# Optimization experiments

Hardware: AMD Instinct MI355X
Metric: run time of the kernel (lower is better)

## Reference

```python
import jax, jax.numpy as jnp
import numpy as np

NUM_CLASSES = 91
NUM_ANCHORS = 3234
VAR_XY, VAR_WH = 0.1, 0.2
SCORE_THRESH = 0.05
NMS_THRESH = 0.5
PRE_NMS_TOPK = 200  # original default 400; reduced to bound the [C-1,K,K] IoU buffer
MAX_DET = 100
BATCH = 64


def _xyxy_to_cxcywh(b):
    wh = b[..., 2:] - b[..., :2]
    c = b[..., :2] + 0.5 * wh
    return jnp.concatenate([c, wh], axis=-1)


def _pairwise_iou(b):
    # b: [K,4] xyxy -> [K,K] IoU
    lt = jnp.maximum(b[:, None, :2], b[None, :, :2])
    rb = jnp.minimum(b[:, None, 2:], b[None, :, 2:])
    inter = jnp.prod(jnp.clip(rb - lt, 0.0), axis=-1)
    area = jnp.prod(jnp.clip(b[:, 2:] - b[:, :2], 0.0), axis=-1)
    union = area[:, None] + area[None, :] - inter
    return inter / jnp.maximum(union, 1e-9)


def _nms_keep(boxes):
    # boxes [K,4] already sorted by descending score; greedy NMS keep mask [K]
    K = boxes.shape[0]
    iou = _pairwise_iou(jax.lax.stop_gradient(boxes))
    idx = jnp.arange(K)

    def body(i, keep):
        suppress = keep[i] & (iou[i] > NMS_THRESH) & (idx > i)
        return keep & ~suppress

    return jax.lax.fori_loop(0, K, body, jnp.ones((K,), dtype=bool))


def setup_inputs() -> dict:
    key = jax.random.key(0)
    k1, k2, k3, k4 = jax.random.split(key, 4)
    cls_logits = jax.random.normal(k1, (BATCH, NUM_ANCHORS, NUM_CLASSES), dtype=jnp.float32)
    box_reg = jax.random.normal(k2, (BATCH, NUM_ANCHORS, 4), dtype=jnp.float32)
    # valid normalized anchor boxes in xyxy
    cxy = jax.random.uniform(k3, (NUM_ANCHORS, 2), minval=0.05, maxval=0.95)
    wh = jax.random.uniform(k4, (NUM_ANCHORS, 2), minval=0.02, maxval=0.4)
    priors = jnp.concatenate([cxy - wh / 2, cxy + wh / 2], axis=-1).astype(jnp.float32)
    return {"cls_logits": cls_logits, "box_reg": box_reg, "priors": priors}


def reference(cls_logits, box_reg, priors):
    probs = jax.nn.softmax(cls_logits, axis=-1)           # [B,A,C]
    pr_c = _xyxy_to_cxcywh(priors)                        # [A,4]

    def per_image(args):
        loc, p = args                                     # [A,4], [A,C]
        # _decode with variances (0.1, 0.2)
        xy = loc[:, :2] * VAR_XY * pr_c[:, 2:] + pr_c[:, :2]
        wh = jnp.exp(loc[:, 2:] * VAR_WH) * pr_c[:, 2:]
        boxes = jnp.concatenate([xy - wh / 2, xy + wh / 2], axis=-1)  # [A,4]

        scores_c = p[:, 1:].T                             # [C-1, A], skip background
        vals, idx = jax.lax.top_k(scores_c, PRE_NMS_TOPK)  # [C-1,K] sorted desc
        boxes_c = boxes[idx]                              # [C-1,K,4]
        keep = jax.vmap(_nms_keep)(boxes_c)               # [C-1,K]
        valid = vals > SCORE_THRESH
        fscores = jnp.where(keep & valid, vals, 0.0)      # masked-out dets scored 0
        labels = jnp.broadcast_to(
            jnp.arange(1, NUM_CLASSES, dtype=jnp.float32)[:, None], fscores.shape)

        flat_s = fscores.reshape(-1)
        flat_b = boxes_c.reshape(-1, 4)
        flat_l = labels.reshape(-1)
        top_s, top_i = jax.lax.top_k(flat_s, MAX_DET)     # global top-100 by score
        preds = jnp.concatenate(
            [flat_b[top_i], top_s[:, None], flat_l[top_i, None]], axis=-1)  # [100,6]
        return jnp.where(top_s[:, None] > 0, preds, 0.0)  # zero padding rows

    return jax.lax.map(per_image, (box_reg, probs))        # [B,100,6]
```

## Files before the change

kernel.cpp:

```cpp
#include <hip/hip_runtime.h>
#include <cstdint>

#define NCLS 91
#define NA   3234
#define NB   64
#define KTOP 200
#define CAP  128
#define MAXDET 100
#define NCM1 90
#define CAPI 8192
#define LCAP 256
#define NBIN 1024
#define BOFF 0x3D4C
#define FBUF 1024
#define PBLK 6468

typedef unsigned long long u64;
typedef unsigned int u32;


__device__ __forceinline__ u64 u64max(u64 a, u64 b) { return a > b ? a : b; }
__device__ __forceinline__ u64 u64min(u64 a, u64 b) { return a < b ? a : b; }

__device__ __forceinline__ u64 shfl_xor_u64(u64 v, int m) {
  int lo = __shfl_xor((int)(u32)v, m, 64);
  int hi = __shfl_xor((int)(u32)(v >> 32), m, 64);
  return ((u64)(u32)hi << 32) | (u32)lo;
}

template <int SLOTS>
__device__ __forceinline__ void bitonic_desc(u64* key, int t) {
  const int N = SLOTS * 64;
  for (int k = 2; k <= N; k <<= 1) {
    for (int j = k >> 1; j > 0; j >>= 1) {
      if (j >= 64) {
        int sj = j >> 6;
        #pragma unroll
        for (int s = 0; s < SLOTS; ++s) {
          int sp = s ^ sj;
          if (sp > s) {
            int e = s * 64 + t;
            bool up = ((e & k) == 0);
            u64 a = key[s], b = key[sp];
            u64 mx = u64max(a, b), mn = u64min(a, b);
            key[s]  = up ? mx : mn;
            key[sp] = up ? mn : mx;
          }
        }
      } else {
        #pragma unroll
        for (int s = 0; s < SLOTS; ++s) {
          int e = s * 64 + t;
          u64 p = shfl_xor_u64(key[s], j);
          bool up = ((e & k) == 0);
          bool lower = ((t & j) == 0);
          key[s] = (up == lower) ? u64max(key[s], p) : u64min(key[s], p);
        }
      }
    }
  }
}

__global__ __launch_bounds__(64) void prep_kernel(
    const float* __restrict__ logits, const float* __restrict__ box_reg,
    const float* __restrict__ priors, float* __restrict__ boxes,
    u64* __restrict__ cand, int* __restrict__ cnt) {
  __shared__ u64 lkey[LCAP];
  __shared__ unsigned short lbc[LCAP];
  __shared__ int lcnt;
  int t = threadIdx.x;
  if (t == 0) lcnt = 0;
  asm volatile("s_waitcnt lgkmcnt(0)" ::: "memory");
  __builtin_amdgcn_sched_barrier(0);

  int half = t & 1;
  int rloc = t >> 1;
  int i = blockIdx.x * 32 + rloc;
  int b = i / NA, a = i - b * NA;

  int F0   = half ? 45 : 0;
  int cntf = half ? 46 : 45;
  const float* lp = logits + (size_t)i * NCLS;
  const float* base = lp + F0;
  int g0 = (int)(((u32)(i * NCLS + F0)) & 3u);
  int lead = (4 - g0) & 3;
  int rem = cntf - lead;
  int n4 = rem >> 2;
  int tail = rem & 3;

  float lv0 = 0.f, lv1 = 0.f, lv2 = 0.f;
  if (lead > 0) lv0 = base[0];
  if (lead > 1) lv1 = base[1];
  if (lead > 2) lv2 = base[2];
  const float4* cv = (const float4*)(base + lead);
  float4 r[11];
  #pragma unroll
  for (int v = 0; v < 10; ++v) r[v] = cv[v];
  r[10] = make_float4(0.f, 0.f, 0.f, 0.f);
  if (n4 > 10) r[10] = cv[10];
  int toff = lead + 4 * n4;
  float tv0 = 0.f, tv1 = 0.f, tv2 = 0.f;
  if (tail > 0) tv0 = base[toff];
  if (tail > 1) tv1 = base[toff + 1];
  if (tail > 2) tv2 = base[toff + 2];

  if (!half) {
    float4 pr = ((const float4*)priors)[a];
    float pw = pr.z - pr.x, ph = pr.w - pr.y;
    float cx = pr.x + 0.5f * pw, cy = pr.y + 0.5f * ph;
    float4 lc = ((const float4*)box_reg)[i];
    float x = lc.x * 0.1f * pw + cx;
    float y = lc.y * 0.1f * ph + cy;
    float bw = expf(lc.z * 0.2f) * pw;
    float bh = expf(lc.w * 0.2f) * ph;
    float4 bxo;
    bxo.x = x - bw * 0.5f; bxo.y = y - bh * 0.5f;
    bxo.z = x + bw * 0.5f; bxo.w = y + bh * 0.5f;
    ((float4*)boxes)[i] = bxo;
  }

  float m = -3.402823466e38f;
  if (lead > 0) m = fmaxf(m, lv0);
  if (lead > 1) m = fmaxf(m, lv1);
  if (lead > 2) m = fmaxf(m, lv2);
  #pragma unroll
  for (int v = 0; v < 10; ++v) {
    float4 q = r[v];
    m = fmaxf(m, fmaxf(fmaxf(q.x, q.y), fmaxf(q.z, q.w)));
  }
  if (n4 > 10) {
    float4 q = r[10];
    m = fmaxf(m, fmaxf(fmaxf(q.x, q.y), fmaxf(q.z, q.w)));
  }
  if (tail > 0) m = fmaxf(m, tv0);
  if (tail > 1) m = fmaxf(m, tv1);
  if (tail > 2) m = fmaxf(m, tv2);
  m = fmaxf(m, __shfl_xor(m, 1, 64));

  auto FOLD = [&](float s) -> float {
    if (lead > 0) s += expf(lv0 - m);
    if (lead > 1) s += expf(lv1 - m);
    if (lead > 2) s += expf(lv2 - m);
    #pragma unroll
    for (int v = 0; v < 10; ++v) {
      float4 q = r[v];
      s += expf(q.x - m); s += expf(q.y - m);
      s += expf(q.z - m); s += expf(q.w - m);
    }
    if (n4 > 10) {
      float4 q = r[10];
      s += expf(q.x - m); s += expf(q.y - m);
      s += expf(q.z - m); s += expf(q.w - m);
    }
    if (tail > 0) s += expf(tv0 - m);
    if (tail > 1) s += expf(tv1 - m);
    if (tail > 2) s += expf(tv2 - m);
    return s;
  };

  float s = 0.f;
  if (!half) s = FOLD(0.f);
  float s_recv = __shfl_xor(s, 1, 64);
  if (half) s = FOLD(s_recv);
  float fin = __shfl_xor(s, 1, 64);
  float ssum = half ? s : fin;

  float lthr = logf(0.05f * ssum);
  u64 abits = (u64)(u32)(~a);
  int bb90 = b * NCM1;
  #define PUSH(L, CC) do { \
    float _d = (L) - m; \
    if (_d > lthr) { \
      float _e = expf(_d); \
      int _lp = atomicAdd(&lcnt, 1); \
      if (_lp < LCAP) { \
        lkey[_lp] = ((u64)__float_as_uint(_e / ssum) << 32) | abits; \
        lbc[_lp] = (unsigned short)(bb90 + (CC) - 1); \
      } \
    } \
  } while (0)

  if (lead > 0 && F0 != 0) PUSH(lv0, F0);
  if (lead > 1) PUSH(lv1, F0 + 1);
  if (lead > 2) PUSH(lv2, F0 + 2);
  {
    int c0 = F0 + lead;
    float4 q = r[0];
    if (c0 != 0) PUSH(q.x, c0);
    PUSH(q.y, c0 + 1); PUSH(q.z, c0 + 2); PUSH(q.w, c0 + 3);
  }
  #pragma unroll
  for (int v = 1; v < 10; ++v) {
    float4 q = r[v];
    int cb = F0 + lead + 4 * v;
    PUSH(q.x, cb); PUSH(q.y, cb + 1); PUSH(q.z, cb + 2); PUSH(q.w, cb + 3);
  }
  if (n4 > 10) {
    float4 q = r[10];
    int cb = F0 + lead + 40;
    PUSH(q.x, cb); PUSH(q.y, cb + 1); PUSH(q.z, cb + 2); PUSH(q.w, cb + 3);
  }
  {
    int cb = F0 + toff;
    if (tail > 0) PUSH(tv0, cb);
    if (tail > 1) PUSH(tv1, cb + 1);
    if (tail > 2) PUSH(tv2, cb + 2);
  }
  #undef PUSH

  asm volatile("s_waitcnt lgkmcnt(0)" ::: "memory");
  __builtin_amdgcn_sched_barrier(0);
  int nL = lcnt; if (nL > LCAP) nL = LCAP;
  for (int j = t; j < nL; j += 64) {
    int bcv = lbc[j];
    int pos = atomicAdd(&cnt[bcv], 1);
    if (pos < CAP) cand[(size_t)bcv * CAP + pos] = lkey[j];
  }
}

__global__ __launch_bounds__(256) void sort_nms_kernel(
    const u64* __restrict__ cand, const int* __restrict__ cnt,
    const float* __restrict__ boxes,
    u64* __restrict__ img_keys, int* __restrict__ img_cnt) {
  __shared__ float4 sbx[4][CAP];
  __shared__ float sar[4][CAP];
  __shared__ u64 sm[4][CAP][2];
  int w = threadIdx.x >> 6;
  int t = threadIdx.x & 63;
  int bc = blockIdx.x * 4 + w;
  int b = bc / NCM1;
  int cm1 = bc - b * NCM1;

  int n = cnt[bc]; if (n > CAP) n = CAP;

  u64 key[2];
  #pragma unroll
  for (int s = 0; s < 2; ++s) {
    int e = s * 64 + t;
    key[s] = (e < n) ? cand[(size_t)bc * CAP + e] : 0ULL;
  }
  if (n <= 64) bitonic_desc<1>(key, t);
  else         bitonic_desc<2>(key, t);

  #pragma unroll
  for (int s = 0; s < 2; ++s) {
    int rr = s * 64 + t;
    if (rr < n) {
      int a = (int)(~(u32)key[s]);
      float4 bbx = ((const float4*)boxes)[b * NA + a];
      sbx[w][rr] = bbx;
      sar[w][rr] = fmaxf(bbx.z - bbx.x, 0.f) * fmaxf(bbx.w - bbx.y, 0.f);
    }
  }
  __syncthreads();

  #pragma unroll
  for (int T = 0; T < 2; ++T) {
    int rr = T * 64 + t;
    float4 bi; float ai = 0.f;
    bool act = (rr < n);
    if (act) { bi = sbx[w][rr]; ai = sar[w][rr]; }
    u64 m0 = 0, m1 = 0;
    for (int j = T * 64 + 1; j < n; ++j) {
      float4 bj = sbx[w][j];
      float aj = sar[w][j];
      if (act && j > rr) {
        float xx1 = fmaxf(bi.x, bj.x), yy1 = fmaxf(bi.y, bj.y);
        float xx2 = fminf(bi.z, bj.z), yy2 = fminf(bi.w, bj.w);
        float inter = fmaxf(xx2 - xx1, 0.f) * fmaxf(yy2 - yy1, 0.f);
        float iou = inter / fmaxf(ai + aj - inter, 1e-9f);
        if (iou > 0.5f) {
          if (j < 64) m0 |= 1ull << j;
          else        m1 |= 1ull << (j - 64);
        }
      }
    }
    if (act) { sm[w][rr][0] = m0; sm[w][rr][1] = m1; }
  }
  __syncthreads();

  u64 kp0 = ~0ull, kp1 = ~0ull;
  for (int i = 0; i < n; ++i) {
    u64 s0 = sm[w][i][0], s1 = sm[w][i][1];
    u64 kw = (i < 64) ? kp0 : kp1;
    u64 live = 0ull - ((kw >> (i & 63)) & 1ull);
    kp0 &= ~(s0 & live); kp1 &= ~(s1 & live);
  }

  auto rng = [](int mm, int wd) -> u64 {
    int c = mm - wd * 64;
    if (c <= 0) return 0ull;
    if (c >= 64) return ~0ull;
    return (1ull << c) - 1ull;
  };
  u64 k0 = kp0 & rng(n, 0), k1 = kp1 & rng(n, 1);
  int c0 = __popcll(k0), c1 = __popcll(k1);
  int tot = c0 + c1;
  int base = 0;
  if (t == 0 && tot) base = atomicAdd(&img_cnt[b], tot);
  base = __shfl(base, 0, 64);
  if (tot) {
    u64 lmlt = (1ull << t) - 1ull;
    u64 kws[2] = {k0, k1};
    int pres[2] = {0, c0};
    #pragma unroll
    for (int s = 0; s < 2; ++s) {
      int rr = s * 64 + t;
      if (rr < n && ((kws[s] >> t) & 1ull)) {
        int pos = base + pres[s] + __popcll(kws[s] & lmlt);
        if (pos < CAPI) {
          u32 sbits = (u32)(key[s] >> 32);
          int fidx = cm1 * KTOP + rr;
          int anch = (int)(~(u32)key[s]);
          img_keys[(size_t)b * CAPI + pos] =
              ((u64)sbits << 27) | ((u64)(u32)(0x7FFF - fidx) << 12) | (u64)(u32)anch;
        }
      }
    }
  }
}

__global__ __launch_bounds__(1024) void topdet_kernel(
    const u64* __restrict__ img_keys, const int* __restrict__ img_cnt,
    const float* __restrict__ boxes, float* __restrict__ out) {
  __shared__ int hist[NBIN];
  __shared__ u64 buf[FBUF];
  __shared__ int sh_nsel, sh_T;
  int b = blockIdx.x, t = threadIdx.x;
  int n = img_cnt[b]; if (n > CAPI) n = CAPI;

  for (int i = t; i < NBIN; i += 1024) hist[i] = 0;
  if (t == 0) { sh_nsel = 0; sh_T = 0; }
  __syncthreads();

  for (int i = t; i < n; i += 1024) {
    int bin = (int)(img_keys[(size_t)b * CAPI + i] >> 43) - BOFF;
    bin = bin < 0 ? 0 : (bin > NBIN - 1 ? NBIN - 1 : bin);
    atomicAdd(&hist[bin], 1);
  }
  __syncthreads();

  if (t < 64) {
    int hi = NBIN - 1 - (t << 4);
    int cs = 0;
    #pragma unroll
    for (int k = 0; k < 16; ++k) cs += hist[hi - k];
    int cum = cs;
    for (int d = 1; d < 64; d <<= 1) {
      int o = __shfl_up(cum, d, 64);
      if (t >= d) cum += o;
    }
    int pre = cum - cs;
    if (pre < MAXDET && cum >= MAXDET) {
      int acc = pre;
      for (int k = 0; k < 16; ++k) {
        acc += hist[hi - k];
        if (acc >= MAXDET) { sh_T = hi - k; break; }
      }
    }
  }
  __syncthreads();

  int T = sh_T;
  for (int i = t; i < n; i += 1024) {
    u64 key = img_keys[(size_t)b * CAPI + i];
    int bin = (int)(key >> 43) - BOFF;
    bin = bin < 0 ? 0 : (bin > NBIN - 1 ? NBIN - 1 : bin);
    if (bin >= T) {
      int pos = atomicAdd(&sh_nsel, 1);
      if (pos < FBUF) buf[pos] = key;
    }
  }
  __syncthreads();

  int ns = sh_nsel; if (ns > FBUF) ns = FBUF;

  if (ns <= 256) {
    if (t < 64) {
      u64 key[4];
      #pragma unroll
      for (int s = 0; s < 4; ++s) {
        int e = s * 64 + t;
        key[s] = (e < ns) ? buf[e] : 0ULL;
      }
      if (ns <= 128) bitonic_desc<2>(key, t);
      else           bitonic_desc<4>(key, t);
      buf[t] = key[0];
      if (t < 36) buf[64 + t] = key[1];
    }
    __syncthreads();
  } else {
    int npow = 1; while (npow < ns) npow <<= 1;
    for (int i = t; i < npow; i += 1024) if (i >= ns) buf[i] = 0ULL;
    __syncthreads();
    for (int k = 2; k <= npow; k <<= 1) {
      for (int j = k >> 1; j > 0; j >>= 1) {
        for (int i = t; i < npow; i += 1024) {
          int l = i ^ j;
          if (l > i) {
            u64 x0 = buf[i], x1 = buf[l];
            bool up = ((i & k) == 0);
            if (up ? (x0 < x1) : (x0 > x1)) { buf[i] = x1; buf[l] = x0; }
          }
        }
        __syncthreads();
      }
    }
  }

  if (t < MAXDET) {
    float* row = out + ((size_t)b * MAXDET + t) * 6;
    if (t < ns) {
      u64 key = buf[t];
      float vsc = __uint_as_float((u32)(key >> 27));
      int fidx = 0x7FFF - (int)((key >> 12) & 0x7FFF);
      int a = (int)(key & 0xFFF);
      float4 bb = ((const float4*)boxes)[b * NA + a];
      row[0] = bb.x; row[1] = bb.y; row[2] = bb.z; row[3] = bb.w;
      row[4] = vsc;
      row[5] = (float)(fidx / KTOP + 1);
    } else {
      row[0] = 0.f; row[1] = 0.f; row[2] = 0.f;
      row[3] = 0.f; row[4] = 0.f; row[5] = 0.f;
    }
  }
}

extern "C" void kernel_launch(void* const* d_in, const int* in_sizes, int n_in,
                              void* d_out, int out_size, void* d_ws, size_t ws_size,
                              hipStream_t stream) {
  const float* logits  = (const float*)d_in[0];
  const float* box_reg = (const float*)d_in[1];
  const float* priors  = (const float*)d_in[2];
  float* out = (float*)d_out;

  char* ws = (char*)d_ws;
  size_t off = 0;
  float* boxes = (float*)(ws + off);               off += (size_t)NB * NA * 4 * sizeof(float);
  u64* cand = (u64*)(ws + off);                    off += (size_t)NB * NCM1 * CAP * sizeof(u64);
  u64* img_keys = (u64*)(ws + off);                off += (size_t)NB * CAPI * sizeof(u64);
  int* cnt = (int*)(ws + off);                     off += (size_t)NB * NCM1 * sizeof(int);
  int* img_cnt = (int*)(ws + off);                 off += (size_t)NB * sizeof(int);
  (void)ws_size; (void)in_sizes; (void)n_in; (void)out_size;

  hipMemsetAsync(cnt, 0, (size_t)(NB * NCM1 + NB) * sizeof(int), stream);
  prep_kernel<<<PBLK, 64, 0, stream>>>(
      logits, box_reg, priors, boxes, cand, cnt);
  sort_nms_kernel<<<NB * NCM1 / 4, 256, 0, stream>>>(
      cand, cnt, boxes, img_keys, img_cnt);
  topdet_kernel<<<NB, 1024, 0, stream>>>(img_keys, img_cnt, boxes, out);
}
```

Before: 225.9 us.

## Stage logits via async global-to-LDS loads, process two slabs per block

The prep kernel now has each 64-thread block handle two 32-anchor slabs. Logits are copied with global_load_lds directly into shared memory, and the second slab's load overlaps processing of the first. Each exp is computed once and reused for both the softmax sum and the candidate push, and box decode is spread across all 64 lanes. The cost is more LDS per block and half as many blocks, which may reduce occupancy and latency hiding. Correctness also relies on the hand-written vmcnt waits being placed right.

```diff
diff --git a/kernel.cpp b/kernel.cpp
--- a/kernel.cpp
+++ b/kernel.cpp
@@ -13,7 +13,6 @@
 #define NBIN 1024
 #define BOFF 0x3D4C
 #define FBUF 1024
-#define PBLK 6468
 
 typedef unsigned long long u64;
 typedef unsigned int u32;
@@ -61,152 +60,190 @@
   }
 }
 
+__device__ __forceinline__ void process_slab(
+    const float* sl, int slab, int t,
+    u64* lkey, unsigned short* lbc, int* lcnt) {
+  int half = t & 1;
+  int r = t >> 1;
+  int i = slab * 32 + r;
+  int b = i / NA, a = i - b * NA;
+
+  int F0 = half ? 45 : 0;
+  int cntf = half ? 46 : 45;
+  const float* base = sl + r * 91 + F0;
+  int g0 = (int)((u32)(r * 91 + F0) & 3u);
+  int lead = (4 - g0) & 3;
+  int rem = cntf - lead;
+  int n4 = rem >> 2;
+  int tail = rem & 3;
+
+  float lv0 = 0.f, lv1 = 0.f, lv2 = 0.f;
+  if (lead > 0) lv0 = base[0];
+  if (lead > 1) lv1 = base[1];
+  if (lead > 2) lv2 = base[2];
+  const float4* cv = (const float4*)(base + lead);
+  float4 r4[11];
+  #pragma unroll
+  for (int v = 0; v < 10; ++v) r4[v] = cv[v];
+  r4[10] = make_float4(0.f, 0.f, 0.f, 0.f);
+  if (n4 > 10) r4[10] = cv[10];
+  int toff = lead + 4 * n4;
+  float tv0 = 0.f, tv1 = 0.f, tv2 = 0.f;
+  if (tail > 0) tv0 = base[toff];
+  if (tail > 1) tv1 = base[toff + 1];
+  if (tail > 2) tv2 = base[toff + 2];
+
+  float m = -3.402823466e38f;
+  if (lead > 0) m = fmaxf(m, lv0);
+  if (lead > 1) m = fmaxf(m, lv1);
+  if (lead > 2) m = fmaxf(m, lv2);
+  #pragma unroll
+  for (int v = 0; v < 10; ++v) {
+    float4 q = r4[v];
+    m = fmaxf(m, fmaxf(fmaxf(q.x, q.y), fmaxf(q.z, q.w)));
+  }
+  if (n4 > 10) {
+    float4 q = r4[10];
+    m = fmaxf(m, fmaxf(fmaxf(q.x, q.y), fmaxf(q.z, q.w)));
+  }
+  if (tail > 0) m = fmaxf(m, tv0);
+  if (tail > 1) m = fmaxf(m, tv1);
+  if (tail > 2) m = fmaxf(m, tv2);
+  m = fmaxf(m, __shfl_xor(m, 1, 64));
+
+  float el0 = expf(lv0 - m), el1 = expf(lv1 - m), el2 = expf(lv2 - m);
+  float4 er[11];
+  #pragma unroll
+  for (int v = 0; v < 11; ++v) {
+    er[v].x = expf(r4[v].x - m);
+    er[v].y = expf(r4[v].y - m);
+    er[v].z = expf(r4[v].z - m);
+    er[v].w = expf(r4[v].w - m);
+  }
+  float et0 = expf(tv0 - m), et1 = expf(tv1 - m), et2 = expf(tv2 - m);
+
+  auto CHAIN = [&](float s) -> float {
+    if (lead > 0) s += el0;
+    if (lead > 1) s += el1;
+    if (lead > 2) s += el2;
+    #pragma unroll
+    for (int v = 0; v < 10; ++v) {
+      s += er[v].x; s += er[v].y; s += er[v].z; s += er[v].w;
+    }
+    if (n4 > 10) { s += er[10].x; s += er[10].y; s += er[10].z; s += er[10].w; }
+    if (tail > 0) s += et0;
+    if (tail > 1) s += et1;
+    if (tail > 2) s += et2;
+    return s;
+  };
+  float s = 0.f;
+  if (!half) s = CHAIN(0.f);
+  float s_recv = __shfl_xor(s, 1, 64);
+  if (half) s = CHAIN(s_recv);
+  float fin = __shfl_xor(s, 1, 64);
+  float ssum = half ? s : fin;
+
+  float lthr = logf(0.05f * ssum);
+  u64 abits = (u64)(u32)(~a);
+  int bb90 = b * NCM1;
+  #define PUSH(L, E, CC) do { \
+    if ((L) - m > lthr) { \
+      float _e = (E); \
+      int _lp = atomicAdd(lcnt, 1); \
+      if (_lp < LCAP) { \
+        lkey[_lp] = ((u64)__float_as_uint(_e / ssum) << 32) | abits; \
+        lbc[_lp] = (unsigned short)(bb90 + (CC) - 1); \
+      } \
+    } \
+  } while (0)
+
+  if (lead > 0 && F0 != 0) PUSH(lv0, el0, F0);
+  if (lead > 1) PUSH(lv1, el1, F0 + 1);
+  if (lead > 2) PUSH(lv2, el2, F0 + 2);
+  {
+    int c0 = F0 + lead;
+    if (c0 != 0) PUSH(r4[0].x, er[0].x, c0);
+    PUSH(r4[0].y, er[0].y, c0 + 1);
+    PUSH(r4[0].z, er[0].z, c0 + 2);
+    PUSH(r4[0].w, er[0].w, c0 + 3);
+  }
+  #pragma unroll
+  for (int v = 1; v < 10; ++v) {
+    int cb = F0 + lead + 4 * v;
+    PUSH(r4[v].x, er[v].x, cb);
+    PUSH(r4[v].y, er[v].y, cb + 1);
+    PUSH(r4[v].z, er[v].z, cb + 2);
+    PUSH(r4[v].w, er[v].w, cb + 3);
+  }
+  if (n4 > 10) {
+    int cb = F0 + lead + 40;
+    PUSH(r4[10].x, er[10].x, cb);
+    PUSH(r4[10].y, er[10].y, cb + 1);
+    PUSH(r4[10].z, er[10].z, cb + 2);
+    PUSH(r4[10].w, er[10].w, cb + 3);
+  }
+  {
+    int cb = F0 + toff;
+    if (tail > 0) PUSH(tv0, et0, cb);
+    if (tail > 1) PUSH(tv1, et1, cb + 1);
+    if (tail > 2) PUSH(tv2, et2, cb + 2);
+  }
+  #undef PUSH
+}
+
 __global__ __launch_bounds__(64) void prep_kernel(
     const float* __restrict__ logits, const float* __restrict__ box_reg,
     const float* __restrict__ priors, float* __restrict__ boxes,
     u64* __restrict__ cand, int* __restrict__ cnt) {
+  __shared__ __align__(16) float sl[2][2912];
   __shared__ u64 lkey[LCAP];
   __shared__ unsigned short lbc[LCAP];
   __shared__ int lcnt;
   int t = threadIdx.x;
   if (t == 0) lcnt = 0;
   asm volatile("s_waitcnt lgkmcnt(0)" ::: "memory");
+
+  int i2 = blockIdx.x * 64 + t;
+  int b2 = i2 / NA, a2 = i2 - b2 * NA;
+  float4 pr = ((const float4*)priors)[a2];
+  float4 lc = ((const float4*)box_reg)[i2];
+
+  #pragma unroll
+  for (int p = 0; p < 2; ++p) {
+    const float* gs = logits + (size_t)(blockIdx.x * 2 + p) * 2912;
+    #pragma unroll
+    for (int k = 0; k < 11; ++k) {
+      __builtin_amdgcn_global_load_lds(
+          (const __attribute__((address_space(1))) void*)(gs + k * 256 + t * 4),
+          (__attribute__((address_space(3))) void*)(&sl[p][k * 256]),
+          16, 0, 0);
+    }
+    if (t < 24) {
+      __builtin_amdgcn_global_load_lds(
+          (const __attribute__((address_space(1))) void*)(gs + 11 * 256 + t * 4),
+          (__attribute__((address_space(3))) void*)(&sl[p][11 * 256]),
+          16, 0, 0);
+    }
+  }
+
+  float pw = pr.z - pr.x, ph = pr.w - pr.y;
+  float cx = pr.x + 0.5f * pw, cy = pr.y + 0.5f * ph;
+  float x = lc.x * 0.1f * pw + cx;
+  float y = lc.y * 0.1f * ph + cy;
+  float bw = expf(lc.z * 0.2f) * pw;
+  float bh = expf(lc.w * 0.2f) * ph;
+  float4 bxo;
+  bxo.x = x - bw * 0.5f; bxo.y = y - bh * 0.5f;
+  bxo.z = x + bw * 0.5f; bxo.w = y + bh * 0.5f;
+  ((float4*)boxes)[i2] = bxo;
+
+  asm volatile("s_waitcnt vmcnt(12)" ::: "memory");
   __builtin_amdgcn_sched_barrier(0);
-
-  int half = t & 1;
-  int rloc = t >> 1;
-  int i = blockIdx.x * 32 + rloc;
-  int b = i / NA, a = i - b * NA;
-
-  int F0   = half ? 45 : 0;
-  int cntf = half ? 46 : 45;
-  const float* lp = logits + (size_t)i * NCLS;
-  const float* base = lp + F0;
-  int g0 = (int)(((u32)(i * NCLS + F0)) & 3u);
-  int lead = (4 - g0) & 3;
-  int rem = cntf - lead;
-  int n4 = rem >> 2;
-  int tail = rem & 3;
-
-  float lv0 = 0.f, lv1 = 0.f, lv2 = 0.f;
-  if (lead > 0) lv0 = base[0];
-  if (lead > 1) lv1 = base[1];
-  if (lead > 2) lv2 = base[2];
-  const float4* cv = (const float4*)(base + lead);
-  float4 r[11];
-  #pragma unroll
-  for (int v = 0; v < 10; ++v) r[v] = cv[v];
-  r[10] = make_float4(0.f, 0.f, 0.f, 0.f);
-  if (n4 > 10) r[10] = cv[10];
-  int toff = lead + 4 * n4;
-  float tv0 = 0.f, tv1 = 0.f, tv2 = 0.f;
-  if (tail > 0) tv0 = base[toff];
-  if (tail > 1) tv1 = base[toff + 1];
-  if (tail > 2) tv2 = base[toff + 2];
-
-  if (!half) {
-    float4 pr = ((const float4*)priors)[a];
-    float pw = pr.z - pr.x, ph = pr.w - pr.y;
-    float cx = pr.x + 0.5f * pw, cy = pr.y + 0.5f * ph;
-    float4 lc = ((const float4*)box_reg)[i];
-    float x = lc.x * 0.1f * pw + cx;
-    float y = lc.y * 0.1f * ph + cy;
-    float bw = expf(lc.z * 0.2f) * pw;
-    float bh = expf(lc.w * 0.2f) * ph;
-    float4 bxo;
-    bxo.x = x - bw * 0.5f; bxo.y = y - bh * 0.5f;
-    bxo.z = x + bw * 0.5f; bxo.w = y + bh * 0.5f;
-    ((float4*)boxes)[i] = bxo;
-  }
-
-  float m = -3.402823466e38f;
-  if (lead > 0) m = fmaxf(m, lv0);
-  if (lead > 1) m = fmaxf(m, lv1);
-  if (lead > 2) m = fmaxf(m, lv2);
-  #pragma unroll
-  for (int v = 0; v < 10; ++v) {
-    float4 q = r[v];
-    m = fmaxf(m, fmaxf(fmaxf(q.x, q.y), fmaxf(q.z, q.w)));
-  }
-  if (n4 > 10) {
-    float4 q = r[10];
-    m = fmaxf(m, fmaxf(fmaxf(q.x, q.y), fmaxf(q.z, q.w)));
-  }
-  if (tail > 0) m = fmaxf(m, tv0);
-  if (tail > 1) m = fmaxf(m, tv1);
-  if (tail > 2) m = fmaxf(m, tv2);
-  m = fmaxf(m, __shfl_xor(m, 1, 64));
-
-  auto FOLD = [&](float s) -> float {
-    if (lead > 0) s += expf(lv0 - m);
-    if (lead > 1) s += expf(lv1 - m);
-    if (lead > 2) s += expf(lv2 - m);
-    #pragma unroll
-    for (int v = 0; v < 10; ++v) {
-      float4 q = r[v];
-      s += expf(q.x - m); s += expf(q.y - m);
-      s += expf(q.z - m); s += expf(q.w - m);
-    }
-    if (n4 > 10) {
-      float4 q = r[10];
-      s += expf(q.x - m); s += expf(q.y - m);
-      s += expf(q.z - m); s += expf(q.w - m);
-    }
-    if (tail > 0) s += expf(tv0 - m);
-    if (tail > 1) s += expf(tv1 - m);
-    if (tail > 2) s += expf(tv2 - m);
-    return s;
-  };
-
-  float s = 0.f;
-  if (!half) s = FOLD(0.f);
-  float s_recv = __shfl_xor(s, 1, 64);
-  if (half) s = FOLD(s_recv);
-  float fin = __shfl_xor(s, 1, 64);
-  float ssum = half ? s : fin;
-
-  float lthr = logf(0.05f * ssum);
-  u64 abits = (u64)(u32)(~a);
-  int bb90 = b * NCM1;
-  #define PUSH(L, CC) do { \
-    float _d = (L) - m; \
-    if (_d > lthr) { \
-      float _e = expf(_d); \
-      int _lp = atomicAdd(&lcnt, 1); \
-      if (_lp < LCAP) { \
-        lkey[_lp] = ((u64)__float_as_uint(_e / ssum) << 32) | abits; \
-        lbc[_lp] = (unsigned short)(bb90 + (CC) - 1); \
-      } \
-    } \
-  } while (0)
-
-  if (lead > 0 && F0 != 0) PUSH(lv0, F0);
-  if (lead > 1) PUSH(lv1, F0 + 1);
-  if (lead > 2) PUSH(lv2, F0 + 2);
-  {
-    int c0 = F0 + lead;
-    float4 q = r[0];
-    if (c0 != 0) PUSH(q.x, c0);
-    PUSH(q.y, c0 + 1); PUSH(q.z, c0 + 2); PUSH(q.w, c0 + 3);
-  }
-  #pragma unroll
-  for (int v = 1; v < 10; ++v) {
-    float4 q = r[v];
-    int cb = F0 + lead + 4 * v;
-    PUSH(q.x, cb); PUSH(q.y, cb + 1); PUSH(q.z, cb + 2); PUSH(q.w, cb + 3);
-  }
-  if (n4 > 10) {
-    float4 q = r[10];
-    int cb = F0 + lead + 40;
-    PUSH(q.x, cb); PUSH(q.y, cb + 1); PUSH(q.z, cb + 2); PUSH(q.w, cb + 3);
-  }
-  {
-    int cb = F0 + toff;
-    if (tail > 0) PUSH(tv0, cb);
-    if (tail > 1) PUSH(tv1, cb + 1);
-    if (tail > 2) PUSH(tv2, cb + 2);
-  }
-  #undef PUSH
+  process_slab(&sl[0][0], blockIdx.x * 2, t, lkey, lbc, &lcnt);
+
+  asm volatile("s_waitcnt vmcnt(0)" ::: "memory");
+  __builtin_amdgcn_sched_barrier(0);
+  process_slab(&sl[1][0], blockIdx.x * 2 + 1, t, lkey, lbc, &lcnt);
 
   asm volatile("s_waitcnt lgkmcnt(0)" ::: "memory");
   __builtin_amdgcn_sched_barrier(0);
@@ -444,7 +481,7 @@
   (void)ws_size; (void)in_sizes; (void)n_in; (void)out_size;
 
   hipMemsetAsync(cnt, 0, (size_t)(NB * NCM1 + NB) * sizeof(int), stream);
-  prep_kernel<<<PBLK, 64, 0, stream>>>(
+  prep_kernel<<<NB * NA / 64, 64, 0, stream>>>(
       logits, box_reg, priors, boxes, cand, cnt);
   sort_nms_kernel<<<NB * NCM1 / 4, 256, 0, stream>>>(
       cand, cnt, boxes, img_keys, img_cnt);
```

After: 239.2 us. 1.06x slower.

## Run per-class greedy NMS wave-locally with shuffles and ballots instead of shared IoU matrix

Applied to the files above, without the earlier changes.

Drops the shared-memory box buffers and the full pairwise IoU bitmask matrix, along with both block barriers, from the sort/NMS kernel. Each lane now keeps its own one or two sorted boxes in registers. The wave walks candidates in score order, broadcasting each still-kept box with shuffles and suppressing later boxes via ballots. Suppressed candidates are skipped entirely, and freeing the shared memory should help occupancy. The trade-off is a serial per-candidate loop of shuffles and divisions instead of fully parallel IoU computation.

```diff
diff --git a/kernel.cpp b/kernel.cpp
--- a/kernel.cpp
+++ b/kernel.cpp
@@ -222,9 +222,6 @@
     const u64* __restrict__ cand, const int* __restrict__ cnt,
     const float* __restrict__ boxes,
     u64* __restrict__ img_keys, int* __restrict__ img_cnt) {
-  __shared__ float4 sbx[4][CAP];
-  __shared__ float sar[4][CAP];
-  __shared__ u64 sm[4][CAP][2];
   int w = threadIdx.x >> 6;
   int t = threadIdx.x & 63;
   int bc = blockIdx.x * 4 + w;
@@ -242,49 +239,18 @@
   if (n <= 64) bitonic_desc<1>(key, t);
   else         bitonic_desc<2>(key, t);
 
-  #pragma unroll
-  for (int s = 0; s < 2; ++s) {
-    int rr = s * 64 + t;
-    if (rr < n) {
-      int a = (int)(~(u32)key[s]);
-      float4 bbx = ((const float4*)boxes)[b * NA + a];
-      sbx[w][rr] = bbx;
-      sar[w][rr] = fmaxf(bbx.z - bbx.x, 0.f) * fmaxf(bbx.w - bbx.y, 0.f);
-    }
-  }
-  __syncthreads();
-
-  #pragma unroll
-  for (int T = 0; T < 2; ++T) {
-    int rr = T * 64 + t;
-    float4 bi; float ai = 0.f;
-    bool act = (rr < n);
-    if (act) { bi = sbx[w][rr]; ai = sar[w][rr]; }
-    u64 m0 = 0, m1 = 0;
-    for (int j = T * 64 + 1; j < n; ++j) {
-      float4 bj = sbx[w][j];
-      float aj = sar[w][j];
-      if (act && j > rr) {
-        float xx1 = fmaxf(bi.x, bj.x), yy1 = fmaxf(bi.y, bj.y);
-        float xx2 = fminf(bi.z, bj.z), yy2 = fminf(bi.w, bj.w);
-        float inter = fmaxf(xx2 - xx1, 0.f) * fmaxf(yy2 - yy1, 0.f);
-        float iou = inter / fmaxf(ai + aj - inter, 1e-9f);
-        if (iou > 0.5f) {
-          if (j < 64) m0 |= 1ull << j;
-          else        m1 |= 1ull << (j - 64);
-        }
-      }
-    }
-    if (act) { sm[w][rr][0] = m0; sm[w][rr][1] = m1; }
-  }
-  __syncthreads();
-
-  u64 kp0 = ~0ull, kp1 = ~0ull;
-  for (int i = 0; i < n; ++i) {
-    u64 s0 = sm[w][i][0], s1 = sm[w][i][1];
-    u64 kw = (i < 64) ? kp0 : kp1;
-    u64 live = 0ull - ((kw >> (i & 63)) & 1ull);
-    kp0 &= ~(s0 & live); kp1 &= ~(s1 & live);
+  float4 bx0 = make_float4(0.f, 0.f, 0.f, 0.f);
+  float4 bx1 = make_float4(0.f, 0.f, 0.f, 0.f);
+  float ar0 = 0.f, ar1 = 0.f;
+  if (t < n) {
+    int a = (int)(~(u32)key[0]);
+    bx0 = ((const float4*)boxes)[b * NA + a];
+    ar0 = fmaxf(bx0.z - bx0.x, 0.f) * fmaxf(bx0.w - bx0.y, 0.f);
+  }
+  if (64 + t < n) {
+    int a = (int)(~(u32)key[1]);
+    bx1 = ((const float4*)boxes)[b * NA + a];
+    ar1 = fmaxf(bx1.z - bx1.x, 0.f) * fmaxf(bx1.w - bx1.y, 0.f);
   }
 
   auto rng = [](int mm, int wd) -> u64 {
@@ -293,7 +259,45 @@
     if (c >= 64) return ~0ull;
     return (1ull << c) - 1ull;
   };
-  u64 k0 = kp0 & rng(n, 0), k1 = kp1 & rng(n, 1);
+  u64 kp0 = rng(n, 0), kp1 = rng(n, 1);
+  bool has1 = (n > 64);
+
+  for (int i = 0; i < n; ++i) {
+    bool hi = i >= 64;
+    u64 kw = hi ? kp1 : kp0;
+    if (!((kw >> (i & 63)) & 1ull)) continue;
+    int src = i & 63;
+    float bix = __shfl(hi ? bx1.x : bx0.x, src, 64);
+    float biy = __shfl(hi ? bx1.y : bx0.y, src, 64);
+    float biz = __shfl(hi ? bx1.z : bx0.z, src, 64);
+    float biw = __shfl(hi ? bx1.w : bx0.w, src, 64);
+    float ai  = __shfl(hi ? ar1 : ar0, src, 64);
+    if (!hi) {
+      float xx1 = fmaxf(bix, bx0.x), yy1 = fmaxf(biy, bx0.y);
+      float xx2 = fminf(biz, bx0.z), yy2 = fminf(biw, bx0.w);
+      float inter = fmaxf(xx2 - xx1, 0.f) * fmaxf(yy2 - yy1, 0.f);
+      float iou = inter / fmaxf(ai + ar0 - inter, 1e-9f);
+      u64 sup0 = __ballot(iou > 0.5f);
+      kp0 &= ~(sup0 & ~((2ull << i) - 1ull));
+      if (has1) {
+        float xx1b = fmaxf(bix, bx1.x), yy1b = fmaxf(biy, bx1.y);
+        float xx2b = fminf(biz, bx1.z), yy2b = fminf(biw, bx1.w);
+        float interb = fmaxf(xx2b - xx1b, 0.f) * fmaxf(yy2b - yy1b, 0.f);
+        float ioub = interb / fmaxf(ai + ar1 - interb, 1e-9f);
+        u64 sup1 = __ballot(ioub > 0.5f);
+        kp1 &= ~sup1;
+      }
+    } else {
+      float xx1b = fmaxf(bix, bx1.x), yy1b = fmaxf(biy, bx1.y);
+      float xx2b = fminf(biz, bx1.z), yy2b = fminf(biw, bx1.w);
+      float interb = fmaxf(xx2b - xx1b, 0.f) * fmaxf(yy2b - yy1b, 0.f);
+      float ioub = interb / fmaxf(ai + ar1 - interb, 1e-9f);
+      u64 sup1 = __ballot(ioub > 0.5f);
+      kp1 &= ~(sup1 & ~((2ull << (i - 64)) - 1ull));
+    }
+  }
+
+  u64 k0 = kp0, k1 = kp1;
   int c0 = __popcll(k0), c1 = __popcll(k1);
   int tot = c0 + c1;
   int base = 0;
```

Result: no change. 224.0 us, median of 2 (-0.8%).
